# Optimization experiments

Measured on AMD Instinct MI355X. Metric: run time of the kernel, lower is better.

## Reference

```python
import jax, jax.numpy as jnp
import numpy as np
from jax import lax

B, CIN, COUT, H, W, K = 8, 64, 64, 96, 96, 3
PAD = K // 2
EPS = 1e-5


def _conv(x, w, pad):
    return lax.conv_general_dilated(x, w, window_strides=(1, 1),
                                    padding=[(pad, pad), (pad, pad)],
                                    dimension_numbers=('NCHW', 'OIHW', 'NCHW'))


def setup_inputs() -> dict:
    key = jax.random.key(0)
    ks = jax.random.split(key, 7)
    x = jax.random.normal(ks[0], (B, CIN, H, W), dtype=jnp.float32)
    # offset conv (zero-init in the original; use small random weights so offsets are nontrivial)
    w_off = jax.random.normal(ks[1], (2 * K * K, CIN, K, K), dtype=jnp.float32) * 0.01
    b_off = jax.random.normal(ks[2], (2 * K * K,), dtype=jnp.float32) * 0.01
    w_def = jax.random.normal(ks[3], (COUT, CIN, K, K), dtype=jnp.float32) * (1.0 / np.sqrt(CIN * K * K))
    b_def = jax.random.normal(ks[4], (COUT,), dtype=jnp.float32) * 0.01
    gamma = jax.random.normal(ks[5], (COUT,), dtype=jnp.float32) * 0.1 + 1.0
    beta = jax.random.normal(ks[6], (COUT,), dtype=jnp.float32) * 0.1
    return {"x": x, "w_off": w_off, "b_off": b_off, "w_def": w_def,
            "b_def": b_def, "gamma": gamma, "beta": beta}


def _deform_block(x, w_off, b_off, w_def, b_def, gamma, beta):
    # 1) predict offsets: [B, 2*K*K, H, W]; channel 2k = dy, 2k+1 = dx for tap k=ky*K+kx
    offset = _conv(x, w_off, PAD) + b_off[None, :, None, None]
    dy = offset[:, 0::2]  # [B, K*K, H, W]
    dx = offset[:, 1::2]

    # 2) sampling positions p = p0 + p_k + dp (stride 1, zero-padding semantics)
    yy = jnp.arange(H, dtype=jnp.float32)[:, None]          # [H,1]
    xx = jnp.arange(W, dtype=jnp.float32)[None, :]          # [1,W]
    kk = jnp.arange(K * K)
    ky = (kk // K - PAD).astype(jnp.float32)[None, :, None, None]
    kx = (kk % K - PAD).astype(jnp.float32)[None, :, None, None]
    py = yy[None, None] + ky + dy                            # [B, K*K, H, W]
    px = xx[None, None] + kx + dx

    # 3) bilinear gather with zero outside-boundary
    y0 = jnp.floor(py); x0 = jnp.floor(px)
    ly = py - y0; lx = px - x0
    x_flat = x.reshape(B, CIN, H * W)
    sampled = jnp.zeros((B, CIN, K * K, H, W), dtype=x.dtype)
    for iy, wy in ((y0, 1.0 - ly), (y0 + 1.0, ly)):
        for ix, wx in ((x0, 1.0 - lx), (x0 + 1.0, lx)):
            valid = (iy >= 0) & (iy < H) & (ix >= 0) & (ix < W)
            yi = jnp.clip(iy, 0, H - 1).astype(jnp.int32)
            xi = jnp.clip(ix, 0, W - 1).astype(jnp.int32)
            idx = (yi * W + xi).reshape(B, -1)               # [B, K*K*H*W]
            vals = jnp.take_along_axis(x_flat, idx[:, None, :], axis=2)
            vals = vals.reshape(B, CIN, K * K, H, W)
            wgt = (wy * wx * valid.astype(x.dtype))[:, None]  # [B,1,K*K,H,W]
            sampled = sampled + vals * wgt

    # 4) deformable conv = contraction of sampled taps with kernel weights
    out = jnp.einsum('bckhw,ock->bohw', sampled, w_def.reshape(COUT, CIN, K * K))
    out = out + b_def[None, :, None, None]

    # 5) BatchNorm (training-mode batch statistics) + ReLU
    mean = jnp.mean(out, axis=(0, 2, 3))
    var = jnp.var(out, axis=(0, 2, 3))
    out = (out - mean[None, :, None, None]) * lax.rsqrt(var + EPS)[None, :, None, None]
    out = out * gamma[None, :, None, None] + beta[None, :, None, None]
    return jax.nn.relu(out)


def reference(x, w_off, b_off, w_def, b_def, gamma, beta):
    return _deform_block(x, w_off, b_off, w_def, b_def, gamma, beta)
```

## Files before the change

### kernel.cpp

```cpp
#include <hip/hip_runtime.h>

#define Hh 96
#define Ww 96
#define CIN 64
#define COUT 64
#define BATCH 8
#define HW 9216
#define NOFF 18

#define XS_ROW   13824
#define XS_SIZE  124416
#define WS_BASE  124416
#define OF_BASE  147744
#define SM_TOTAL 159264

typedef __attribute__((ext_vector_type(8))) short bf16x8;
typedef __attribute__((ext_vector_type(4))) float f32x4;

__device__ inline ushort f2bf(float f) {
  union { float f; uint u; } v; v.f = f;
  uint u = v.u;
  u += 0x7FFF + ((u >> 16) & 1);
  return (ushort)(u >> 16);
}
__device__ inline float bf2f(ushort s) {
  union { uint u; float f; } v; v.u = ((uint)s) << 16; return v.f;
}
__device__ inline float bflo(uint u) {
  union { uint u; float f; } v; v.u = u << 16; return v.f;
}
__device__ inline float bfhi(uint u) {
  union { uint u; float f; } v; v.u = u & 0xFFFF0000u; return v.f;
}
__device__ inline uint pack_rne(float a, float b) {
  union { float f; uint u; } x, y; x.f = a; y.f = b;
  uint ua = x.u + (0x7FFFu + ((x.u >> 16) & 1));
  uint ub = y.u + (0x7FFFu + ((y.u >> 16) & 1));
  return (ua >> 16) | (ub & 0xFFFF0000u);
}
__device__ inline uint interp_pack(uint p00, uint p01, uint p10, uint p11,
                                   float w00, float w01, float w10, float w11) {
  float vlo = fmaf(w11, bflo(p11), fmaf(w10, bflo(p10),
              fmaf(w01, bflo(p01), w00 * bflo(p00))));
  float vhi = fmaf(w11, bfhi(p11), fmaf(w10, bfhi(p10),
              fmaf(w01, bfhi(p01), w00 * bfhi(p00))));
  return pack_rne(vlo, vhi);
}

__global__ __launch_bounds__(256) void k_xt(
    const float* __restrict__ x, const float* __restrict__ w_def,
    const float* __restrict__ w_off, ushort* __restrict__ xt,
    ushort* __restrict__ wtb, ushort* __restrict__ wob)
{
  __shared__ float tile[64][65];
  int tid = threadIdx.x;
  int blk = blockIdx.x;

  if (blk < 9) {
    for (int i = tid; i < 4096; i += 256) {
      int o = i >> 6, c = i & 63;
      wtb[blk * 4096 + i] = f2bf(w_def[(o * 64 + c) * 9 + blk]);
    }
  } else if (blk < 25 && blk >= 16) {
    int k = blk - 16;
    for (int i = tid; i < 2048; i += 256) {
      int n = i >> 6, c = i & 63;
      wob[k * 2048 + i] = (n < NOFF) ? f2bf(w_off[(n * 64 + c) * 9 + k]) : (ushort)0;
    }
  }

  int b = blk / 144;
  int pbase = (blk - b * 144) * 64;
  int wave = tid >> 6, lane = tid & 63;
  const float* xp = x + (size_t)b * CIN * HW + pbase;
  #pragma unroll
  for (int i = 0; i < 16; ++i) {
    int c = wave * 16 + i;
    tile[lane][c] = xp[(size_t)c * HW + lane];
  }
  __syncthreads();
  ushort* xo = xt + ((size_t)b * HW + pbase) * 64;
  #pragma unroll
  for (int i = 0; i < 16; ++i) {
    int p = wave * 16 + i;
    xo[(size_t)p * 64 + lane] = f2bf(tile[p][lane]);
  }
}

__global__ __launch_bounds__(512, 2) void k_main(
    const ushort* __restrict__ xt, const ushort* __restrict__ wtb,
    const ushort* __restrict__ wob, const float* __restrict__ b_off,
    const float* __restrict__ b_def, float* __restrict__ out,
    float* __restrict__ parts)
{
  extern __shared__ char sm[];
  int tid = threadIdx.x;
  int bid = blockIdx.x;
  int b = bid & 7;
  int rt = bid >> 3;
  int r0 = rt * 3;

  {
    const ushort* xsrc = xt + (size_t)b * HW * 64;
    for (int q = tid; q < 6912; q += 512) {
      int s = q / 768;
      int rem = q - s * 768;
      int cxp = rem >> 3, c16 = rem & 7;
      int srow = min(max(r0 - 3 + s, 0), 95);
      uint4 v = *(const uint4*)(xsrc + (size_t)(srow * 96 + cxp) * 64 + c16 * 8);
      *(uint4*)(sm + s * XS_ROW + cxp * 144 + c16 * 16) = v;
    }
  }
  for (int q = tid; q < 1296; q += 512) {
    int k = q / 144;
    int rem = q - k * 144;
    int n = rem >> 3, c16 = rem & 7;
    uint4 v = *(const uint4*)(wob + k * 2048 + n * 64 + c16 * 8);
    *(uint4*)(sm + WS_BASE + k * 2592 + n * 144 + c16 * 16) = v;
  }
  __syncthreads();

  int wave = tid >> 6, lane = tid & 63;
  int m = lane & 15, hi = lane >> 4;
  int kh = wave & 1;
  int gb = wave >> 1;
  int khB = kh * 64, hiB = hi * 16;

  int hA[5], wAc[5], pPix[5], gV[5];
  #pragma unroll
  for (int ti = 0; ti < 5; ++ti) {
    int g = gb + ti * 4;
    gV[ti] = g;
    int gr = g / 6, gc = g - gr * 6;
    hA[ti] = r0 + gr;
    wAc[ti] = gc * 16 + m;
    pPix[ti] = g * 16 + m;
  }

  f32x4 oacc[5][2];
  #pragma unroll
  for (int ti = 0; ti < 5; ++ti) {
    oacc[ti][0] = (f32x4){0.f, 0.f, 0.f, 0.f};
    oacc[ti][1] = (f32x4){0.f, 0.f, 0.f, 0.f};
  }
  for (int k = 0; k < 9; ++k) {
    int ky = k / 3 - 1, kx = (k - (k / 3) * 3) - 1;
    const char* wkb = sm + WS_BASE + k * 2592;
    bf16x8 wb0 = *(const bf16x8*)(wkb + m * 144 + hiB + khB);
    int r1 = min(16 + m, 17);
    bf16x8 wb1 = *(const bf16x8*)(wkb + r1 * 144 + hiB + khB);
    #pragma unroll
    for (int ti = 0; ti < 5; ++ti) {
      if (gV[ti] < 18) {
        int yy = hA[ti] + ky, xx = wAc[ti] + kx;
        bool valid = (yy >= 0 && yy < Hh && xx >= 0 && xx < Ww);
        int cy = min(max(yy, 0), 95), cx = min(max(xx, 0), 95);
        int sy = cy - r0 + 3;
        bf16x8 a = *(const bf16x8*)(sm + sy * XS_ROW + cx * 144 + hiB + khB);
        if (!valid) a = (bf16x8)0;
        oacc[ti][0] = __builtin_amdgcn_mfma_f32_16x16x32_bf16(a, wb0, oacc[ti][0], 0, 0, 0);
        oacc[ti][1] = __builtin_amdgcn_mfma_f32_16x16x32_bf16(a, wb1, oacc[ti][1], 0, 0, 0);
      }
    }
  }

  int j0 = m, j1 = 16 + m;
  if (kh == 1) {
    #pragma unroll
    for (int ti = 0; ti < 5; ++ti) {
      if (gV[ti] < 18) {
        #pragma unroll
        for (int r = 0; r < 4; ++r) {
          int p = gV[ti] * 16 + hi * 4 + r;
          *(ushort*)(sm + OF_BASE + p * 40 + j0 * 2) = f2bf(oacc[ti][0][r]);
          if (m < 2)
            *(ushort*)(sm + OF_BASE + p * 40 + j1 * 2) = f2bf(oacc[ti][1][r]);
        }
      }
    }
  }
  __syncthreads();
  if (kh == 0) {
    float bo0 = b_off[j0];
    float bo1 = (m < 2) ? b_off[j1] : 0.f;
    #pragma unroll
    for (int ti = 0; ti < 5; ++ti) {
      if (gV[ti] < 18) {
        #pragma unroll
        for (int r = 0; r < 4; ++r) {
          int p = gV[ti] * 16 + hi * 4 + r;
          ushort* a0p = (ushort*)(sm + OF_BASE + p * 40 + j0 * 2);
          *a0p = f2bf(oacc[ti][0][r] + bf2f(*a0p) + bo0);
          if (m < 2) {
            ushort* a1p = (ushort*)(sm + OF_BASE + p * 40 + j1 * 2);
            *a1p = f2bf(oacc[ti][1][r] + bf2f(*a1p) + bo1);
          }
        }
      }
    }
  }
  {
    int o = tid >> 3, c16 = tid & 7;
    uint4 v = *(const uint4*)(wtb + o * 64 + c16 * 8);
    *(uint4*)(sm + WS_BASE + o * 144 + c16 * 16) = v;
  }
  __syncthreads();

  f32x4 acc[5][4];
  #pragma unroll
  for (int ti = 0; ti < 5; ++ti)
    #pragma unroll
    for (int nt = 0; nt < 4; ++nt) acc[ti][nt] = (f32x4){0.f, 0.f, 0.f, 0.f};

  for (int k = 0; k < 9; ++k) {
    if (k < 8) {
      int o = tid >> 3, c16 = tid & 7;
      uint4 v = *(const uint4*)(wtb + (k + 1) * 4096 + o * 64 + c16 * 8);
      *(uint4*)(sm + WS_BASE + ((k + 1) & 1) * 9216 + o * 144 + c16 * 16) = v;
    }
    int ky = k / 3 - 1, kx = (k - (k / 3) * 3) - 1;
    const char* wkb = sm + WS_BASE + (k & 1) * 9216;
    bf16x8 bf0 = *(const bf16x8*)(wkb + m * 144 + hiB + khB);
    bf16x8 bf1 = *(const bf16x8*)(wkb + (16 + m) * 144 + hiB + khB);
    bf16x8 bf2 = *(const bf16x8*)(wkb + (32 + m) * 144 + hiB + khB);
    bf16x8 bf3 = *(const bf16x8*)(wkb + (48 + m) * 144 + hiB + khB);

    #pragma unroll
    for (int ti = 0; ti < 5; ++ti) {
      if (gV[ti] < 18) {
        uint dd = *(const uint*)(sm + OF_BASE + pPix[ti] * 40 + k * 4);
        float dy = bflo(dd), dx = bfhi(dd);
        float py = (float)(hA[ti] + ky) + dy;
        float px = (float)(wAc[ti] + kx) + dx;
        float y0f = floorf(py), x0f = floorf(px);
        float ly = py - y0f, lx = px - x0f;
        int y0 = (int)y0f, x0 = (int)x0f;
        int y1 = y0 + 1, x1 = x0 + 1;
        float fy0 = (y0 >= 0 && y0 < Hh) ? 1.f : 0.f;
        float fy1 = (y1 >= 0 && y1 < Hh) ? 1.f : 0.f;
        float fx0 = (x0 >= 0 && x0 < Ww) ? 1.f : 0.f;
        float fx1 = (x1 >= 0 && x1 < Ww) ? 1.f : 0.f;
        int cy0 = min(max(y0, 0), 95), cy1 = min(max(y1, 0), 95);
        int cx0 = min(max(x0, 0), 95), cx1 = min(max(x1, 0), 95);
        int sy0 = min(max(cy0 - r0 + 3, 0), 8);
        int sy1 = min(max(cy1 - r0 + 3, 0), 8);
        const char* row0 = sm + sy0 * XS_ROW;
        const char* row1 = sm + sy1 * XS_ROW;
        uint4 c00 = *(const uint4*)(row0 + cx0 * 144 + hiB + khB);
        uint4 c01 = *(const uint4*)(row0 + cx1 * 144 + hiB + khB);
        uint4 c10 = *(const uint4*)(row1 + cx0 * 144 + hiB + khB);
        uint4 c11 = *(const uint4*)(row1 + cx1 * 144 + hiB + khB);
        float w00 = (1.f - ly) * (1.f - lx) * (fy0 * fx0);
        float w01 = (1.f - ly) * lx * (fy0 * fx1);
        float w10 = ly * (1.f - lx) * (fy1 * fx0);
        float w11 = ly * lx * (fy1 * fx1);
        uint ua[4];
        ua[0] = interp_pack(c00.x, c01.x, c10.x, c11.x, w00, w01, w10, w11);
        ua[1] = interp_pack(c00.y, c01.y, c10.y, c11.y, w00, w01, w10, w11);
        ua[2] = interp_pack(c00.z, c01.z, c10.z, c11.z, w00, w01, w10, w11);
        ua[3] = interp_pack(c00.w, c01.w, c10.w, c11.w, w00, w01, w10, w11);
        bf16x8 av;
        __builtin_memcpy(&av, ua, 16);
        acc[ti][0] = __builtin_amdgcn_mfma_f32_16x16x32_bf16(av, bf0, acc[ti][0], 0, 0, 0);
        acc[ti][1] = __builtin_amdgcn_mfma_f32_16x16x32_bf16(av, bf1, acc[ti][1], 0, 0, 0);
        acc[ti][2] = __builtin_amdgcn_mfma_f32_16x16x32_bf16(av, bf2, acc[ti][2], 0, 0, 0);
        acc[ti][3] = __builtin_amdgcn_mfma_f32_16x16x32_bf16(av, bf3, acc[ti][3], 0, 0, 0);
      }
    }
    __syncthreads();
  }

  float* T = (float*)sm;
  {
    float bd[4];
    bd[0] = b_def[m]; bd[1] = b_def[16 + m];
    bd[2] = b_def[32 + m]; bd[3] = b_def[48 + m];
    #pragma unroll
    for (int ti = 0; ti < 5; ++ti) {
      if (gV[ti] < 18) {
        #pragma unroll
        for (int nt = 0; nt < 4; ++nt) {
          int o = nt * 16 + m;
          #pragma unroll
          for (int r = 0; r < 4; ++r) {
            int p = gV[ti] * 16 + hi * 4 + r;
            if (kh == 1) T[o * 289 + p] = acc[ti][nt][r];
          }
        }
      }
    }
  }
  __syncthreads();
  if (kh == 0) {
    float bd[4];
    bd[0] = b_def[m]; bd[1] = b_def[16 + m];
    bd[2] = b_def[32 + m]; bd[3] = b_def[48 + m];
    #pragma unroll
    for (int ti = 0; ti < 5; ++ti) {
      if (gV[ti] < 18) {
        #pragma unroll
        for (int nt = 0; nt < 4; ++nt) {
          int o = nt * 16 + m;
          #pragma unroll
          for (int r = 0; r < 4; ++r) {
            int p = gV[ti] * 16 + hi * 4 + r;
            T[o * 289 + p] += acc[ti][nt][r] + bd[nt];
          }
        }
      }
    }
  }
  __syncthreads();
  {
    int o = tid >> 3, seg = tid & 7;
    const float* Tr = T + o * 289 + seg * 36;
    float* og = out + ((size_t)(b * 64 + o)) * HW + rt * 288 + seg * 36;
    float s = 0.f, ss = 0.f;
    #pragma unroll
    for (int j4 = 0; j4 < 9; ++j4) {
      float4 v;
      v.x = Tr[j4 * 4 + 0]; v.y = Tr[j4 * 4 + 1];
      v.z = Tr[j4 * 4 + 2]; v.w = Tr[j4 * 4 + 3];
      s += v.x + v.y + v.z + v.w;
      ss += v.x * v.x + v.y * v.y + v.z * v.z + v.w * v.w;
      *(float4*)(og + j4 * 4) = v;
    }
    s += __shfl_down(s, 4); s += __shfl_down(s, 2); s += __shfl_down(s, 1);
    ss += __shfl_down(ss, 4); ss += __shfl_down(ss, 2); ss += __shfl_down(ss, 1);
    if ((tid & 7) == 0) {
      parts[o * 256 + bid] = s;
      parts[16384 + o * 256 + bid] = ss;
    }
  }
}

__global__ __launch_bounds__(256) void k_stats(
    const float* __restrict__ parts, const float* __restrict__ gamma,
    const float* __restrict__ beta, float* __restrict__ stats)
{
  int c = blockIdx.x;
  int tid = threadIdx.x;
  float s = 0.f, ss = 0.f;
  for (int i = tid; i < 256; i += 256) {
    s += parts[c * 256 + i];
    ss += parts[16384 + c * 256 + i];
  }
  #pragma unroll
  for (int off = 32; off >= 1; off >>= 1) {
    s += __shfl_down(s, off);
    ss += __shfl_down(ss, off);
  }
  __shared__ float rs[4], rss[4];
  int wave = tid >> 6, lane = tid & 63;
  if (lane == 0) { rs[wave] = s; rss[wave] = ss; }
  __syncthreads();
  if (tid == 0) {
    float S1 = rs[0] + rs[1] + rs[2] + rs[3];
    float S2 = rss[0] + rss[1] + rss[2] + rss[3];
    const float inv = 1.f / 73728.f;
    float mean = S1 * inv;
    float var = S2 * inv - mean * mean;
    float scale = gamma[c] * rsqrtf(var + 1e-5f);
    stats[c] = scale;
    stats[64 + c] = beta[c] - mean * scale;
  }
}

__global__ __launch_bounds__(256) void k_norm(
    float* __restrict__ out, const float* __restrict__ stats)
{
  int g = blockIdx.x * 256 + threadIdx.x;
  int o = (g / 2304) & 63;
  float sc = stats[o], sh = stats[64 + o];
  float4 v = ((const float4*)out)[g];
  v.x = fmaxf(fmaf(v.x, sc, sh), 0.f);
  v.y = fmaxf(fmaf(v.y, sc, sh), 0.f);
  v.z = fmaxf(fmaf(v.z, sc, sh), 0.f);
  v.w = fmaxf(fmaf(v.w, sc, sh), 0.f);
  ((float4*)out)[g] = v;
}

extern "C" void kernel_launch(void* const* d_in, const int* in_sizes, int n_in,
                              void* d_out, int out_size, void* d_ws, size_t ws_size,
                              hipStream_t stream) {
  const float* x     = (const float*)d_in[0];
  const float* w_off = (const float*)d_in[1];
  const float* b_off = (const float*)d_in[2];
  const float* w_def = (const float*)d_in[3];
  const float* b_def = (const float*)d_in[4];
  const float* gamma = (const float*)d_in[5];
  const float* beta  = (const float*)d_in[6];
  float* out = (float*)d_out;

  float* base  = (float*)d_ws;
  ushort* wtb  = (ushort*)base;
  ushort* wob  = (ushort*)(base + 18432);
  ushort* xt   = (ushort*)(base + 18432 + 9216);
  float* parts = base + 18432 + 9216 + 2359296;
  float* stats = parts + 32768;

  static bool attr_set = false;
  (void)hipFuncSetAttribute((const void*)k_main,
      hipFuncAttributeMaxDynamicSharedMemorySize, SM_TOTAL);

  k_xt<<<1152, 256, 0, stream>>>(x, w_def, w_off, xt, wtb, wob);
  k_main<<<256, 512, SM_TOTAL, stream>>>(xt, wtb, wob, b_off, b_def, out, parts);
  k_stats<<<64, 256, 0, stream>>>(parts, gamma, beta, stats);
  k_norm<<<4608, 256, 0, stream>>>(out, stats);
}
```

Before: 66.95 us.

## Use 12 waves per block in deformable conv kernel and hardware bf16 pack

Grows the main kernel from 8 to 12 waves per block, so each wave pair handles exactly 3 of the 18 pixel groups instead of up to 5 with idle guarded iterations. This balances the MFMA and bilinear-gather work across waves and removes the gV<18 branches. Weight staging and the output stores are restricted to the first 512 threads. Separately, the manual round-to-nearest bf16 packing in the interpolation is replaced by the v_cvt_pk_bf16_f32 instruction. The larger block lowers the per-thread register budget, with launch bounds (768,3) that a 159KB shared-memory block cannot reach anyway, so spills are a risk.

```diff
diff --git a/kernel.cpp b/kernel.cpp
--- a/kernel.cpp
+++ b/kernel.cpp
@@ -32,11 +32,10 @@
 __device__ inline float bfhi(uint u) {
   union { uint u; float f; } v; v.u = u & 0xFFFF0000u; return v.f;
 }
-__device__ inline uint pack_rne(float a, float b) {
-  union { float f; uint u; } x, y; x.f = a; y.f = b;
-  uint ua = x.u + (0x7FFFu + ((x.u >> 16) & 1));
-  uint ub = y.u + (0x7FFFu + ((y.u >> 16) & 1));
-  return (ua >> 16) | (ub & 0xFFFF0000u);
+__device__ inline uint cvtpk(float lo, float hi) {
+  uint r;
+  asm("v_cvt_pk_bf16_f32 %0, %1, %2" : "=v"(r) : "v"(lo), "v"(hi));
+  return r;
 }
 __device__ inline uint interp_pack(uint p00, uint p01, uint p10, uint p11,
                                    float w00, float w01, float w10, float w11) {
@@ -44,7 +43,7 @@
               fmaf(w01, bflo(p01), w00 * bflo(p00))));
   float vhi = fmaf(w11, bfhi(p11), fmaf(w10, bfhi(p10),
               fmaf(w01, bfhi(p01), w00 * bfhi(p00))));
-  return pack_rne(vlo, vhi);
+  return cvtpk(vlo, vhi);
 }
 
 __global__ __launch_bounds__(256) void k_xt(
@@ -87,7 +86,7 @@
   }
 }
 
-__global__ __launch_bounds__(512, 2) void k_main(
+__global__ __launch_bounds__(768, 3) void k_main(
     const ushort* __restrict__ xt, const ushort* __restrict__ wtb,
     const ushort* __restrict__ wob, const float* __restrict__ b_off,
     const float* __restrict__ b_def, float* __restrict__ out,
@@ -102,7 +101,7 @@
 
   {
     const ushort* xsrc = xt + (size_t)b * HW * 64;
-    for (int q = tid; q < 6912; q += 512) {
+    for (int q = tid; q < 6912; q += 768) {
       int s = q / 768;
       int rem = q - s * 768;
       int cxp = rem >> 3, c16 = rem & 7;
@@ -111,7 +110,7 @@
       *(uint4*)(sm + s * XS_ROW + cxp * 144 + c16 * 16) = v;
     }
   }
-  for (int q = tid; q < 1296; q += 512) {
+  for (int q = tid; q < 1296; q += 768) {
     int k = q / 144;
     int rem = q - k * 144;
     int n = rem >> 3, c16 = rem & 7;
@@ -126,10 +125,10 @@
   int gb = wave >> 1;
   int khB = kh * 64, hiB = hi * 16;
 
-  int hA[5], wAc[5], pPix[5], gV[5];
-  #pragma unroll
-  for (int ti = 0; ti < 5; ++ti) {
-    int g = gb + ti * 4;
+  int hA[3], wAc[3], pPix[3], gV[3];
+  #pragma unroll
+  for (int ti = 0; ti < 3; ++ti) {
+    int g = gb + ti * 6;
     gV[ti] = g;
     int gr = g / 6, gc = g - gr * 6;
     hA[ti] = r0 + gr;
@@ -137,9 +136,9 @@
     pPix[ti] = g * 16 + m;
   }
 
-  f32x4 oacc[5][2];
-  #pragma unroll
-  for (int ti = 0; ti < 5; ++ti) {
+  f32x4 oacc[3][2];
+  #pragma unroll
+  for (int ti = 0; ti < 3; ++ti) {
     oacc[ti][0] = (f32x4){0.f, 0.f, 0.f, 0.f};
     oacc[ti][1] = (f32x4){0.f, 0.f, 0.f, 0.f};
   }
@@ -150,32 +149,28 @@
     int r1 = min(16 + m, 17);
     bf16x8 wb1 = *(const bf16x8*)(wkb + r1 * 144 + hiB + khB);
     #pragma unroll
-    for (int ti = 0; ti < 5; ++ti) {
-      if (gV[ti] < 18) {
-        int yy = hA[ti] + ky, xx = wAc[ti] + kx;
-        bool valid = (yy >= 0 && yy < Hh && xx >= 0 && xx < Ww);
-        int cy = min(max(yy, 0), 95), cx = min(max(xx, 0), 95);
-        int sy = cy - r0 + 3;
-        bf16x8 a = *(const bf16x8*)(sm + sy * XS_ROW + cx * 144 + hiB + khB);
-        if (!valid) a = (bf16x8)0;
-        oacc[ti][0] = __builtin_amdgcn_mfma_f32_16x16x32_bf16(a, wb0, oacc[ti][0], 0, 0, 0);
-        oacc[ti][1] = __builtin_amdgcn_mfma_f32_16x16x32_bf16(a, wb1, oacc[ti][1], 0, 0, 0);
-      }
+    for (int ti = 0; ti < 3; ++ti) {
+      int yy = hA[ti] + ky, xx = wAc[ti] + kx;
+      bool valid = (yy >= 0 && yy < Hh && xx >= 0 && xx < Ww);
+      int cy = min(max(yy, 0), 95), cx = min(max(xx, 0), 95);
+      int sy = cy - r0 + 3;
+      bf16x8 a = *(const bf16x8*)(sm + sy * XS_ROW + cx * 144 + hiB + khB);
+      if (!valid) a = (bf16x8)0;
+      oacc[ti][0] = __builtin_amdgcn_mfma_f32_16x16x32_bf16(a, wb0, oacc[ti][0], 0, 0, 0);
+      oacc[ti][1] = __builtin_amdgcn_mfma_f32_16x16x32_bf16(a, wb1, oacc[ti][1], 0, 0, 0);
     }
   }
 
   int j0 = m, j1 = 16 + m;
   if (kh == 1) {
     #pragma unroll
-    for (int ti = 0; ti < 5; ++ti) {
-      if (gV[ti] < 18) {
-        #pragma unroll
-        for (int r = 0; r < 4; ++r) {
-          int p = gV[ti] * 16 + hi * 4 + r;
-          *(ushort*)(sm + OF_BASE + p * 40 + j0 * 2) = f2bf(oacc[ti][0][r]);
-          if (m < 2)
-            *(ushort*)(sm + OF_BASE + p * 40 + j1 * 2) = f2bf(oacc[ti][1][r]);
-        }
+    for (int ti = 0; ti < 3; ++ti) {
+      #pragma unroll
+      for (int r = 0; r < 4; ++r) {
+        int p = gV[ti] * 16 + hi * 4 + r;
+        *(ushort*)(sm + OF_BASE + p * 40 + j0 * 2) = f2bf(oacc[ti][0][r]);
+        if (m < 2)
+          *(ushort*)(sm + OF_BASE + p * 40 + j1 * 2) = f2bf(oacc[ti][1][r]);
       }
     }
   }
@@ -184,36 +179,34 @@
     float bo0 = b_off[j0];
     float bo1 = (m < 2) ? b_off[j1] : 0.f;
     #pragma unroll
-    for (int ti = 0; ti < 5; ++ti) {
-      if (gV[ti] < 18) {
-        #pragma unroll
-        for (int r = 0; r < 4; ++r) {
-          int p = gV[ti] * 16 + hi * 4 + r;
-          ushort* a0p = (ushort*)(sm + OF_BASE + p * 40 + j0 * 2);
-          *a0p = f2bf(oacc[ti][0][r] + bf2f(*a0p) + bo0);
-          if (m < 2) {
-            ushort* a1p = (ushort*)(sm + OF_BASE + p * 40 + j1 * 2);
-            *a1p = f2bf(oacc[ti][1][r] + bf2f(*a1p) + bo1);
-          }
+    for (int ti = 0; ti < 3; ++ti) {
+      #pragma unroll
+      for (int r = 0; r < 4; ++r) {
+        int p = gV[ti] * 16 + hi * 4 + r;
+        ushort* a0p = (ushort*)(sm + OF_BASE + p * 40 + j0 * 2);
+        *a0p = f2bf(oacc[ti][0][r] + bf2f(*a0p) + bo0);
+        if (m < 2) {
+          ushort* a1p = (ushort*)(sm + OF_BASE + p * 40 + j1 * 2);
+          *a1p = f2bf(oacc[ti][1][r] + bf2f(*a1p) + bo1);
         }
       }
     }
   }
-  {
+  if (tid < 512) {
     int o = tid >> 3, c16 = tid & 7;
     uint4 v = *(const uint4*)(wtb + o * 64 + c16 * 8);
     *(uint4*)(sm + WS_BASE + o * 144 + c16 * 16) = v;
   }
   __syncthreads();
 
-  f32x4 acc[5][4];
-  #pragma unroll
-  for (int ti = 0; ti < 5; ++ti)
+  f32x4 acc[3][4];
+  #pragma unroll
+  for (int ti = 0; ti < 3; ++ti)
     #pragma unroll
     for (int nt = 0; nt < 4; ++nt) acc[ti][nt] = (f32x4){0.f, 0.f, 0.f, 0.f};
 
   for (int k = 0; k < 9; ++k) {
-    if (k < 8) {
+    if (k < 8 && tid < 512) {
       int o = tid >> 3, c16 = tid & 7;
       uint4 v = *(const uint4*)(wtb + (k + 1) * 4096 + o * 64 + c16 * 8);
       *(uint4*)(sm + WS_BASE + ((k + 1) & 1) * 9216 + o * 144 + c16 * 16) = v;
@@ -226,69 +219,61 @@
     bf16x8 bf3 = *(const bf16x8*)(wkb + (48 + m) * 144 + hiB + khB);
 
     #pragma unroll
-    for (int ti = 0; ti < 5; ++ti) {
-      if (gV[ti] < 18) {
-        uint dd = *(const uint*)(sm + OF_BASE + pPix[ti] * 40 + k * 4);
-        float dy = bflo(dd), dx = bfhi(dd);
-        float py = (float)(hA[ti] + ky) + dy;
-        float px = (float)(wAc[ti] + kx) + dx;
-        float y0f = floorf(py), x0f = floorf(px);
-        float ly = py - y0f, lx = px - x0f;
-        int y0 = (int)y0f, x0 = (int)x0f;
-        int y1 = y0 + 1, x1 = x0 + 1;
-        float fy0 = (y0 >= 0 && y0 < Hh) ? 1.f : 0.f;
-        float fy1 = (y1 >= 0 && y1 < Hh) ? 1.f : 0.f;
-        float fx0 = (x0 >= 0 && x0 < Ww) ? 1.f : 0.f;
-        float fx1 = (x1 >= 0 && x1 < Ww) ? 1.f : 0.f;
-        int cy0 = min(max(y0, 0), 95), cy1 = min(max(y1, 0), 95);
-        int cx0 = min(max(x0, 0), 95), cx1 = min(max(x1, 0), 95);
-        int sy0 = min(max(cy0 - r0 + 3, 0), 8);
-        int sy1 = min(max(cy1 - r0 + 3, 0), 8);
-        const char* row0 = sm + sy0 * XS_ROW;
-        const char* row1 = sm + sy1 * XS_ROW;
-        uint4 c00 = *(const uint4*)(row0 + cx0 * 144 + hiB + khB);
-        uint4 c01 = *(const uint4*)(row0 + cx1 * 144 + hiB + khB);
-        uint4 c10 = *(const uint4*)(row1 + cx0 * 144 + hiB + khB);
-        uint4 c11 = *(const uint4*)(row1 + cx1 * 144 + hiB + khB);
-        float w00 = (1.f - ly) * (1.f - lx) * (fy0 * fx0);
-        float w01 = (1.f - ly) * lx * (fy0 * fx1);
-        float w10 = ly * (1.f - lx) * (fy1 * fx0);
-        float w11 = ly * lx * (fy1 * fx1);
-        uint ua[4];
-        ua[0] = interp_pack(c00.x, c01.x, c10.x, c11.x, w00, w01, w10, w11);
-        ua[1] = interp_pack(c00.y, c01.y, c10.y, c11.y, w00, w01, w10, w11);
-        ua[2] = interp_pack(c00.z, c01.z, c10.z, c11.z, w00, w01, w10, w11);
-        ua[3] = interp_pack(c00.w, c01.w, c10.w, c11.w, w00, w01, w10, w11);
-        bf16x8 av;
-        __builtin_memcpy(&av, ua, 16);
-        acc[ti][0] = __builtin_amdgcn_mfma_f32_16x16x32_bf16(av, bf0, acc[ti][0], 0, 0, 0);
-        acc[ti][1] = __builtin_amdgcn_mfma_f32_16x16x32_bf16(av, bf1, acc[ti][1], 0, 0, 0);
-        acc[ti][2] = __builtin_amdgcn_mfma_f32_16x16x32_bf16(av, bf2, acc[ti][2], 0, 0, 0);
-        acc[ti][3] = __builtin_amdgcn_mfma_f32_16x16x32_bf16(av, bf3, acc[ti][3], 0, 0, 0);
-      }
+    for (int ti = 0; ti < 3; ++ti) {
+      uint dd = *(const uint*)(sm + OF_BASE + pPix[ti] * 40 + k * 4);
+      float dy = bflo(dd), dx = bfhi(dd);
+      float py = (float)(hA[ti] + ky) + dy;
+      float px = (float)(wAc[ti] + kx) + dx;
+      float y0f = floorf(py), x0f = floorf(px);
+      float ly = py - y0f, lx = px - x0f;
+      int y0 = (int)y0f, x0 = (int)x0f;
+      int y1 = y0 + 1, x1 = x0 + 1;
+      float fy0 = (y0 >= 0 && y0 < Hh) ? 1.f : 0.f;
+      float fy1 = (y1 >= 0 && y1 < Hh) ? 1.f : 0.f;
+      float fx0 = (x0 >= 0 && x0 < Ww) ? 1.f : 0.f;
+      float fx1 = (x1 >= 0 && x1 < Ww) ? 1.f : 0.f;
+      int cy0 = min(max(y0, 0), 95), cy1 = min(max(y1, 0), 95);
+      int cx0 = min(max(x0, 0), 95), cx1 = min(max(x1, 0), 95);
+      int sy0 = min(max(cy0 - r0 + 3, 0), 8);
+      int sy1 = min(max(cy1 - r0 + 3, 0), 8);
+      const char* row0 = sm + sy0 * XS_ROW;
+      const char* row1 = sm + sy1 * XS_ROW;
+      uint4 c00 = *(const uint4*)(row0 + cx0 * 144 + hiB + khB);
+      uint4 c01 = *(const uint4*)(row0 + cx1 * 144 + hiB + khB);
+      uint4 c10 = *(const uint4*)(row1 + cx0 * 144 + hiB + khB);
+      uint4 c11 = *(const uint4*)(row1 + cx1 * 144 + hiB + khB);
+      float w00 = (1.f - ly) * (1.f - lx) * (fy0 * fx0);
+      float w01 = (1.f - ly) * lx * (fy0 * fx1);
+      float w10 = ly * (1.f - lx) * (fy1 * fx0);
+      float w11 = ly * lx * (fy1 * fx1);
+      uint ua[4];
+      ua[0] = interp_pack(c00.x, c01.x, c10.x, c11.x, w00, w01, w10, w11);
+      ua[1] = interp_pack(c00.y, c01.y, c10.y, c11.y, w00, w01, w10, w11);
+      ua[2] = interp_pack(c00.z, c01.z, c10.z, c11.z, w00, w01, w10, w11);
+      ua[3] = interp_pack(c00.w, c01.w, c10.w, c11.w, w00, w01, w10, w11);
+      bf16x8 av;
+      __builtin_memcpy(&av, ua, 16);
+      acc[ti][0] = __builtin_amdgcn_mfma_f32_16x16x32_bf16(av, bf0, acc[ti][0], 0, 0, 0);
+      acc[ti][1] = __builtin_amdgcn_mfma_f32_16x16x32_bf16(av, bf1, acc[ti][1], 0, 0, 0);
+      acc[ti][2] = __builtin_amdgcn_mfma_f32_16x16x32_bf16(av, bf2, acc[ti][2], 0, 0, 0);
+      acc[ti][3] = __builtin_amdgcn_mfma_f32_16x16x32_bf16(av, bf3, acc[ti][3], 0, 0, 0);
     }
     __syncthreads();
   }
 
   float* T = (float*)sm;
-  {
-    float bd[4];
-    bd[0] = b_def[m]; bd[1] = b_def[16 + m];
-    bd[2] = b_def[32 + m]; bd[3] = b_def[48 + m];
-    #pragma unroll
-    for (int ti = 0; ti < 5; ++ti) {
-      if (gV[ti] < 18) {
+  if (kh == 1) {
+    #pragma unroll
+    for (int ti = 0; ti < 3; ++ti)
+      #pragma unroll
+      for (int nt = 0; nt < 4; ++nt) {
+        int o = nt * 16 + m;
         #pragma unroll
-        for (int nt = 0; nt < 4; ++nt) {
-          int o = nt * 16 + m;
-          #pragma unroll
-          for (int r = 0; r < 4; ++r) {
-            int p = gV[ti] * 16 + hi * 4 + r;
-            if (kh == 1) T[o * 289 + p] = acc[ti][nt][r];
-          }
+        for (int r = 0; r < 4; ++r) {
+          int p = gV[ti] * 16 + hi * 4 + r;
+          T[o * 289 + p] = acc[ti][nt][r];
         }
       }
-    }
   }
   __syncthreads();
   if (kh == 0) {
@@ -296,22 +281,19 @@
     bd[0] = b_def[m]; bd[1] = b_def[16 + m];
     bd[2] = b_def[32 + m]; bd[3] = b_def[48 + m];
     #pragma unroll
-    for (int ti = 0; ti < 5; ++ti) {
-      if (gV[ti] < 18) {
+    for (int ti = 0; ti < 3; ++ti)
+      #pragma unroll
+      for (int nt = 0; nt < 4; ++nt) {
+        int o = nt * 16 + m;
         #pragma unroll
-        for (int nt = 0; nt < 4; ++nt) {
-          int o = nt * 16 + m;
-          #pragma unroll
-          for (int r = 0; r < 4; ++r) {
-            int p = gV[ti] * 16 + hi * 4 + r;
-            T[o * 289 + p] += acc[ti][nt][r] + bd[nt];
-          }
+        for (int r = 0; r < 4; ++r) {
+          int p = gV[ti] * 16 + hi * 4 + r;
+          T[o * 289 + p] += acc[ti][nt][r] + bd[nt];
         }
       }
-    }
-  }
-  __syncthreads();
-  {
+  }
+  __syncthreads();
+  if (tid < 512) {
     int o = tid >> 3, seg = tid & 7;
     const float* Tr = T + o * 289 + seg * 36;
     float* og = out + ((size_t)(b * 64 + o)) * HW + rt * 288 + seg * 36;
@@ -399,12 +381,11 @@
   float* parts = base + 18432 + 9216 + 2359296;
   float* stats = parts + 32768;
 
-  static bool attr_set = false;
   (void)hipFuncSetAttribute((const void*)k_main,
       hipFuncAttributeMaxDynamicSharedMemorySize, SM_TOTAL);
 
   k_xt<<<1152, 256, 0, stream>>>(x, w_def, w_off, xt, wtb, wob);
-  k_main<<<256, 512, SM_TOTAL, stream>>>(xt, wtb, wob, b_off, b_def, out, parts);
+  k_main<<<256, 768, SM_TOTAL, stream>>>(xt, wtb, wob, b_off, b_def, out, parts);
   k_stats<<<64, 256, 0, stream>>>(parts, gamma, beta, stats);
   k_norm<<<4608, 256, 0, stream>>>(out, stats);
 }
```

Result: faster. 59.95 us (median of 2 runs) (-10.5%).
